# Optimization experiments

Hardware: AMD Instinct MI355X
Metric: run time of the kernel (lower is better)

Reference implementation:

```python
import jax, jax.numpy as jnp
import numpy as np

NUM_HEADS = 8  # attention_head_size = C // NUM_HEADS, used only for score scaling


def conv1x1(x, w, b):
    # x: [B, Cin, H, W], w: [Cout, Cin], b: [Cout]
    return jnp.einsum('bchw,oc->bohw', x, w) + b[None, :, None, None]


def setup_inputs() -> dict:
    key = jax.random.key(0)
    ks = jax.random.split(key, 10)
    B, C, H, W = 8, 256, 96, 96
    x = jax.random.normal(ks[0], (B, C, H, W), dtype=jnp.float32)
    y = jax.random.normal(ks[1], (B, 1, 24, 24), dtype=jnp.float32)
    s = 0.02
    wy = jax.random.normal(ks[2], (C, 1), dtype=jnp.float32) * s
    by = jnp.zeros((C,), dtype=jnp.float32)
    wq = jax.random.normal(ks[3], (C, C), dtype=jnp.float32) * s
    bq = jnp.zeros((C,), dtype=jnp.float32)
    wk = jax.random.normal(ks[4], (C, C), dtype=jnp.float32) * s
    bk = jnp.zeros((C,), dtype=jnp.float32)
    wv = jax.random.normal(ks[5], (C, C), dtype=jnp.float32) * s
    bv = jnp.zeros((C,), dtype=jnp.float32)
    return {'x': x, 'y': y, 'wy': wy, 'by': by, 'wq': wq, 'bq': bq,
            'wk': wk, 'bk': bk, 'wv': wv, 'bv': bv}


def reference(x, y, wy, by, wq, bq, wk, bk, wv, bv):
    B, C, H, W = x.shape
    head_size = C // NUM_HEADS
    # x branch
    xq = conv1x1(x, wq, bq)
    xk = conv1x1(x, wk, bk)
    v = conv1x1(x, wv, bv)
    # y branch: 1 -> C channels, bilinear upsample (align_corners=False == half-pixel)
    y2 = conv1x1(y, wy, by)
    y2 = jax.image.resize(y2, (B, C, H, W), method='bilinear')
    yq = conv1x1(y2, wq, bq)
    yk = conv1x1(y2, wk, bk)
    # gated Q/K
    q = (xq * yq).transpose(0, 2, 1, 3)  # [B, H, C, W]
    k = (xk * yk).transpose(0, 2, 1, 3)
    vt = v.transpose(0, 2, 1, 3)
    # channel attention per spatial row: scores [B, H, C, C]
    scores = jnp.einsum('bhcw,bhdw->bhcd', q, k) / jnp.sqrt(jnp.asarray(head_size, x.dtype))
    probs = jax.nn.softmax(scores, axis=-1)
    out = jnp.einsum('bhcd,bhdw->bhcw', probs, vt)
    return out.transpose(0, 2, 1, 3)  # [B, C, H, W]
```

## Files before the change

kernel.cpp:

```cpp
#include <hip/hip_runtime.h>

typedef __bf16 bf16;
typedef __attribute__((ext_vector_type(8))) __bf16 bf16x8;
typedef __attribute__((ext_vector_type(4))) __bf16 bf16x4;
typedef __attribute__((ext_vector_type(4))) float f32x4;

#define MFMA16(A, B, C) __builtin_amdgcn_mfma_f32_16x16x32_bf16(A, B, C, 0, 0, 0)

__global__ __launch_bounds__(256) void k_prep(
    const float* __restrict__ y, const float* __restrict__ wy, const float* __restrict__ by,
    const float* __restrict__ wq, const float* __restrict__ bq,
    const float* __restrict__ wk, const float* __restrict__ bk,
    const float* __restrict__ wv,
    bf16* __restrict__ wq_bf, bf16* __restrict__ wk_bf, bf16* __restrict__ wv_bf,
    float* __restrict__ yu, float* __restrict__ aq, float* __restrict__ cq,
    float* __restrict__ ak, float* __restrict__ ck)
{
  int blk = blockIdx.x, t = threadIdx.x;
  if (blk < 192) {
    int idx4 = blk * 256 + t;
    int fo = idx4 * 4;
    const float* src; bf16* dst; int off;
    if (fo < 65536)       { src = wq; dst = wq_bf; off = fo; }
    else if (fo < 131072) { src = wk; dst = wk_bf; off = fo - 65536; }
    else                  { src = wv; dst = wv_bf; off = fo - 131072; }
    float4 v = *(const float4*)(src + off);
    bf16x4 o;
    o[0] = (bf16)v.x; o[1] = (bf16)v.y; o[2] = (bf16)v.z; o[3] = (bf16)v.w;
    *(bf16x4*)(dst + off) = o;
  } else if (blk < 200) {
    int b = blk - 192;
    const float* yb = y + b * 576;
#pragma unroll 1
    for (int i = 0; i < 36; ++i) {
      int e = t + i * 256;
      int oh = e / 96, ow = e % 96;
      float sh = oh * 0.25f - 0.375f;
      float sw = ow * 0.25f - 0.375f;
      int ih0 = (int)floorf(sh);
      int iw0 = (int)floorf(sw);
      float fh = sh - (float)ih0, fw = sw - (float)iw0;
      int ih0c = min(23, max(0, ih0)), ih1c = min(23, max(0, ih0 + 1));
      int iw0c = min(23, max(0, iw0)), iw1c = min(23, max(0, iw0 + 1));
      float v00 = yb[ih0c * 24 + iw0c], v01 = yb[ih0c * 24 + iw1c];
      float v10 = yb[ih1c * 24 + iw0c], v11 = yb[ih1c * 24 + iw1c];
      yu[b * 9216 + e] = (1.0f - fh) * ((1.0f - fw) * v00 + fw * v01)
                       + fh * ((1.0f - fw) * v10 + fw * v11);
    }
  } else {
    int ol = t >> 5, cl = t & 31;
    int o = (blk - 200) * 8 + ol;
    int c0 = cl * 8;
    float4 wy0 = *(const float4*)(wy + c0), wy1 = *(const float4*)(wy + c0 + 4);
    float4 by0 = *(const float4*)(by + c0), by1 = *(const float4*)(by + c0 + 4);
    float4 q0  = *(const float4*)(wq + o * 256 + c0), q1 = *(const float4*)(wq + o * 256 + c0 + 4);
    float4 k0  = *(const float4*)(wk + o * 256 + c0), k1 = *(const float4*)(wk + o * 256 + c0 + 4);
    float wyv[8] = {wy0.x, wy0.y, wy0.z, wy0.w, wy1.x, wy1.y, wy1.z, wy1.w};
    float byv[8] = {by0.x, by0.y, by0.z, by0.w, by1.x, by1.y, by1.z, by1.w};
    float qv[8]  = {q0.x, q0.y, q0.z, q0.w, q1.x, q1.y, q1.z, q1.w};
    float kv[8]  = {k0.x, k0.y, k0.z, k0.w, k1.x, k1.y, k1.z, k1.w};
    float saq = 0.f, scq = 0.f, sak = 0.f, sck = 0.f;
#pragma unroll
    for (int j = 0; j < 8; ++j) {
      saq += qv[j] * wyv[j]; scq += qv[j] * byv[j];
      sak += kv[j] * wyv[j]; sck += kv[j] * byv[j];
    }
#pragma unroll
    for (int s = 16; s >= 1; s >>= 1) {
      saq += __shfl_xor(saq, s, 32);
      scq += __shfl_xor(scq, s, 32);
      sak += __shfl_xor(sak, s, 32);
      sck += __shfl_xor(sck, s, 32);
    }
    if (cl == 0) {
      aq[o] = saq; cq[o] = scq + bq[o];
      ak[o] = sak; ck[o] = sck + bk[o];
    }
  }
}

__global__ __launch_bounds__(1024, 1) void k_fused(
    const float* __restrict__ x, const float* __restrict__ yu,
    const bf16* __restrict__ wq_bf, const bf16* __restrict__ wk_bf, const bf16* __restrict__ wv_bf,
    const float* __restrict__ bq, const float* __restrict__ bk, const float* __restrict__ bv,
    const float* __restrict__ aq, const float* __restrict__ cq,
    const float* __restrict__ ak, const float* __restrict__ ck,
    float* __restrict__ out)
{
  __shared__ __align__(16) bf16 xs[96 * 264];
  __shared__ __align__(16) bf16 ks[256 * 104];

  int pl = blockIdx.x;
  int b = pl / 96, h = pl % 96;
  int t = threadIdx.x;
  int wid = t >> 6, lane = t & 63;
  int l15 = lane & 15, g = lane >> 4;
  int otile = wid * 16;

  {
    const float* xrow = x + (size_t)b * 2359296 + (size_t)h * 96;
#pragma unroll
    for (int i = 0; i < 3; ++i) {
      int tsk = i * 1024 + t;
      int w = tsk % 96;
      int c0 = (tsk / 96) * 8;
      float v[8];
#pragma unroll
      for (int j = 0; j < 8; ++j) v[j] = xrow[(size_t)(c0 + j) * 9216 + w];
      bf16x8 o8;
#pragma unroll
      for (int j = 0; j < 8; ++j) o8[j] = (bf16)v[j];
      *(bf16x8*)(xs + w * 264 + c0) = o8;
    }
  }

  size_t wo0 = (size_t)(otile + l15) * 256 + g * 8;
  bf16x8 Bq_c = *(const bf16x8*)(wq_bf + wo0);
  bf16x8 Bk_c = *(const bf16x8*)(wk_bf + wo0);
  bf16x8 Bv_c = *(const bf16x8*)(wv_bf + wo0);

  __syncthreads();

  const float SC = 0.17677669529663687f;

  bf16x8 qf[3];

  {
    f32x4 qacc[6] = {};
    f32x4 kacc[6] = {};
    f32x4 vacc[6] = {};
#pragma unroll 1
    for (int kq = 0; kq < 8; ++kq) {
      bf16x8 Bq_n, Bk_n, Bv_n;
      if (kq < 7) {
        size_t wo = wo0 + (kq + 1) * 32;
        Bq_n = *(const bf16x8*)(wq_bf + wo);
        Bk_n = *(const bf16x8*)(wk_bf + wo);
        Bv_n = *(const bf16x8*)(wv_bf + wo);
      }
      const bf16* xp = xs + kq * 32 + g * 8;
      bf16x8 A[6];
#pragma unroll
      for (int m = 0; m < 6; ++m)
        A[m] = *(const bf16x8*)(xp + (m * 16 + l15) * 264);
#pragma unroll
      for (int m = 0; m < 6; ++m) {
        qacc[m] = MFMA16(A[m], Bq_c, qacc[m]);
        kacc[m] = MFMA16(A[m], Bk_c, kacc[m]);
        vacc[m] = MFMA16(Bv_c, A[m], vacc[m]);
      }
      Bq_c = Bq_n; Bk_c = Bk_n; Bv_c = Bv_n;
    }

    float4 yv[6];
    {
      const float* yr = yu + (size_t)pl * 96;
#pragma unroll
      for (int mt = 0; mt < 6; ++mt)
        yv[mt] = *(const float4*)(yr + mt * 16 + g * 4);
    }
    int o = otile + l15;
    float bqv = bq[o], aq0 = aq[o], cq0 = cq[o];
    float bkv = bk[o], ak0 = ak[o], ck0 = ck[o];

#pragma unroll
    for (int kk = 0; kk < 3; ++kk) {
      bf16x8 qq;
#pragma unroll
      for (int jh = 0; jh < 2; ++jh) {
        int m = 2 * kk + jh;
        float yy[4] = {yv[m].x, yv[m].y, yv[m].z, yv[m].w};
#pragma unroll
        for (int r = 0; r < 4; ++r)
          qq[jh * 4 + r] = (bf16)((qacc[m][r] + bqv) * (yy[r] * aq0 + cq0) * SC);
      }
      qf[kk] = qq;
    }

#pragma unroll
    for (int m = 0; m < 6; ++m) {
      float yy[4] = {yv[m].x, yv[m].y, yv[m].z, yv[m].w};
      bf16x4 pk;
#pragma unroll
      for (int r = 0; r < 4; ++r)
        pk[r] = (bf16)((kacc[m][r] + bkv) * (yy[r] * ak0 + ck0));
      *(bf16x4*)(ks + (size_t)o * 104 + m * 16 + g * 4) = pk;
    }

    float4 bm = *(const float4*)(bv + otile + g * 4);
    float bb[4] = {bm.x, bm.y, bm.z, bm.w};
    __syncthreads();
    bf16* vs = xs;
    int vbase = (otile & ~16) + ((otile >> 2) & 4);
#pragma unroll
    for (int n = 0; n < 6; ++n) {
      bf16x4 pk;
#pragma unroll
      for (int r = 0; r < 4; ++r) pk[r] = (bf16)(vacc[n][r] + bb[r]);
      *(bf16x4*)(vs + (size_t)(n * 16 + l15) * 264 + vbase + g * 8) = pk;
    }
  }
  __syncthreads();

  const bf16* vs = xs;
  f32x4 oacc[6] = {};
  float lp = 0.f;

  auto load_K = [&](int dt, bf16x8* K) {
    const bf16* kp = ks + (size_t)(dt * 32 + l15) * 104 + g * 4;
#pragma unroll
    for (int kk = 0; kk < 3; ++kk)
#pragma unroll
      for (int dn = 0; dn < 2; ++dn) {
        const bf16* p = kp + (size_t)(dn * 16) * 104 + kk * 32;
        bf16x4 lo = *(const bf16x4*)(p);
        bf16x4 hi = *(const bf16x4*)(p + 16);
        K[kk * 2 + dn] = __builtin_shufflevector(lo, hi, 0, 1, 2, 3, 4, 5, 6, 7);
      }
  };

  bf16x8 KA[6], KB[6];
  load_K(0, KA);

  auto attn_step = [&](int dt, bf16x8* Kc, bf16x8* Kn, bool pf) {
    int d0 = dt * 32;
    if (pf) load_K(dt + 1, Kn);
    f32x4 s0 = {}, s1 = {};
    __builtin_amdgcn_s_setprio(1);
#pragma unroll
    for (int kk = 0; kk < 3; ++kk) {
      s0 = MFMA16(Kc[kk * 2 + 0], qf[kk], s0);
      s1 = MFMA16(Kc[kk * 2 + 1], qf[kk], s1);
    }
    __builtin_amdgcn_s_setprio(0);
    bf16x8 pa;
#pragma unroll
    for (int r = 0; r < 4; ++r) {
      float e0 = __expf(s0[r]);
      float e1 = __expf(s1[r]);
      lp += e0 + e1;
      pa[r] = (bf16)e0;
      pa[4 + r] = (bf16)e1;
    }
    const bf16* vp = vs + (size_t)l15 * 264 + d0 + g * 8;
    __builtin_amdgcn_s_setprio(1);
#pragma unroll
    for (int n = 0; n < 6; ++n) {
      bf16x8 Bv = *(const bf16x8*)(vp + (size_t)n * 16 * 264);
      oacc[n] = MFMA16(pa, Bv, oacc[n]);
    }
    __builtin_amdgcn_s_setprio(0);
  };

#pragma unroll 1
  for (int dt2 = 0; dt2 < 4; ++dt2) {
    attn_step(2 * dt2,     KA, KB, true);
    attn_step(2 * dt2 + 1, KB, KA, 2 * dt2 + 1 < 7);
  }

  float vsum = lp;
  vsum += __shfl_xor(vsum, 16, 64);
  vsum += __shfl_xor(vsum, 32, 64);
  float inv = 1.0f / vsum;
  float invr[4];
#pragma unroll
  for (int r = 0; r < 4; ++r)
    invr[r] = __shfl(inv, g * 4 + r, 16);

  float* ob = out + (size_t)b * 2359296 + (size_t)h * 96;
#pragma unroll
  for (int n = 0; n < 6; ++n) {
    int w = n * 16 + l15;
#pragma unroll
    for (int r = 0; r < 4; ++r) {
      int o = otile + g * 4 + r;
      ob[(size_t)o * 9216 + w] = oacc[n][r] * invr[r];
    }
  }
}

extern "C" void kernel_launch(void* const* d_in, const int* in_sizes, int n_in,
                              void* d_out, int out_size, void* d_ws, size_t ws_size,
                              hipStream_t stream) {
  const float* x  = (const float*)d_in[0];
  const float* y  = (const float*)d_in[1];
  const float* wy = (const float*)d_in[2];
  const float* by = (const float*)d_in[3];
  const float* wq = (const float*)d_in[4];
  const float* bq = (const float*)d_in[5];
  const float* wk = (const float*)d_in[6];
  const float* bk = (const float*)d_in[7];
  const float* wv = (const float*)d_in[8];
  const float* bv = (const float*)d_in[9];
  float* out = (float*)d_out;

  char* wsb = (char*)d_ws;
  bf16* wq_bf = (bf16*)(wsb);
  bf16* wk_bf = (bf16*)(wsb + 131072);
  bf16* wv_bf = (bf16*)(wsb + 262144);
  float* yu   = (float*)(wsb + 393216);
  float* aq   = (float*)(wsb + 688128);
  float* cq   = (float*)(wsb + 689152);
  float* ak   = (float*)(wsb + 690176);
  float* ck   = (float*)(wsb + 691200);

  hipLaunchKernelGGL(k_prep, dim3(232), dim3(256), 0, stream,
                     y, wy, by, wq, bq, wk, bk, wv,
                     wq_bf, wk_bf, wv_bf, yu, aq, cq, ak, ck);
  hipLaunchKernelGGL(k_fused, dim3(768), dim3(1024), 0, stream,
                     x, yu, wq_bf, wk_bf, wv_bf, bq, bk, bv,
                     aq, cq, ak, ck, out);
}
```

Baseline: 216.2 us.

## Split x-row staging into halves to overlap global loads with first MFMAs

The fused kernel now loads only the first 128 input channels of the x row into LDS before starting the projection MFMAs. Loads for the second half are issued into registers and stay in flight while the first four k-steps run, then get converted and stored to LDS after a barrier. This hides part of the global-load latency of the strided x gather, at the cost of extra registers in a kernel that already runs one 1024-thread block per CU. The prep kernel is also reshaped so weight conversion does two vectors per thread and the bilinear upsample is spread over 96 blocks instead of 8.

```diff
diff --git a/kernel.cpp b/kernel.cpp
--- a/kernel.cpp
+++ b/kernel.cpp
@@ -17,23 +17,27 @@
     float* __restrict__ ak, float* __restrict__ ck)
 {
   int blk = blockIdx.x, t = threadIdx.x;
-  if (blk < 192) {
-    int idx4 = blk * 256 + t;
-    int fo = idx4 * 4;
-    const float* src; bf16* dst; int off;
-    if (fo < 65536)       { src = wq; dst = wq_bf; off = fo; }
-    else if (fo < 131072) { src = wk; dst = wk_bf; off = fo - 65536; }
-    else                  { src = wv; dst = wv_bf; off = fo - 131072; }
-    float4 v = *(const float4*)(src + off);
-    bf16x4 o;
-    o[0] = (bf16)v.x; o[1] = (bf16)v.y; o[2] = (bf16)v.z; o[3] = (bf16)v.w;
-    *(bf16x4*)(dst + off) = o;
-  } else if (blk < 200) {
-    int b = blk - 192;
+  if (blk < 96) {
+#pragma unroll
+    for (int rep = 0; rep < 2; ++rep) {
+      int idx4 = rep * 24576 + blk * 256 + t;
+      int fo = idx4 * 4;
+      const float* src; bf16* dst; int off;
+      if (fo < 65536)       { src = wq; dst = wq_bf; off = fo; }
+      else if (fo < 131072) { src = wk; dst = wk_bf; off = fo - 65536; }
+      else                  { src = wv; dst = wv_bf; off = fo - 131072; }
+      float4 v = *(const float4*)(src + off);
+      bf16x4 o;
+      o[0] = (bf16)v.x; o[1] = (bf16)v.y; o[2] = (bf16)v.z; o[3] = (bf16)v.w;
+      *(bf16x4*)(dst + off) = o;
+    }
+  } else if (blk < 192) {
+    int blkc = blk - 96;
+    int b = blkc / 12, seg = blkc % 12;
     const float* yb = y + b * 576;
-#pragma unroll 1
-    for (int i = 0; i < 36; ++i) {
-      int e = t + i * 256;
+#pragma unroll
+    for (int i = 0; i < 3; ++i) {
+      int e = seg * 768 + i * 256 + t;
       int oh = e / 96, ow = e % 96;
       float sh = oh * 0.25f - 0.375f;
       float sw = ow * 0.25f - 0.375f;
@@ -49,7 +53,7 @@
     }
   } else {
     int ol = t >> 5, cl = t & 31;
-    int o = (blk - 200) * 8 + ol;
+    int o = (blk - 192) * 8 + ol;
     int c0 = cl * 8;
     float4 wy0 = *(const float4*)(wy + c0), wy1 = *(const float4*)(wy + c0 + 4);
     float4 by0 = *(const float4*)(by + c0), by1 = *(const float4*)(by + c0 + 4);
@@ -97,13 +101,14 @@
   int l15 = lane & 15, g = lane >> 4;
   int otile = wid * 16;
 
-  {
-    const float* xrow = x + (size_t)b * 2359296 + (size_t)h * 96;
-#pragma unroll
-    for (int i = 0; i < 3; ++i) {
-      int tsk = i * 1024 + t;
-      int w = tsk % 96;
-      int c0 = (tsk / 96) * 8;
+  const float* xrow = x + (size_t)b * 2359296 + (size_t)h * 96;
+
+#pragma unroll
+  for (int rep = 0; rep < 2; ++rep) {
+    int task = rep * 1024 + t;
+    if (task < 1536) {
+      int w = task % 96;
+      int c0 = (task / 96) * 8;
       float v[8];
 #pragma unroll
       for (int j = 0; j < 8; ++j) v[j] = xrow[(size_t)(c0 + j) * 9216 + w];
@@ -129,8 +134,57 @@
     f32x4 qacc[6] = {};
     f32x4 kacc[6] = {};
     f32x4 vacc[6] = {};
+
+    float vB0[8], vB1[8];
+    int wB0 = t % 96, cB0 = (t / 96) * 8 + 128;
+#pragma unroll
+    for (int j = 0; j < 8; ++j) vB0[j] = xrow[(size_t)(cB0 + j) * 9216 + wB0];
+    int tB1 = 1024 + t;
+    int wB1 = tB1 % 96, cB1 = (tB1 / 96) * 8 + 128;
+    if (t < 512) {
+#pragma unroll
+      for (int j = 0; j < 8; ++j) vB1[j] = xrow[(size_t)(cB1 + j) * 9216 + wB1];
+    }
+
 #pragma unroll 1
-    for (int kq = 0; kq < 8; ++kq) {
+    for (int kq = 0; kq < 4; ++kq) {
+      bf16x8 Bq_n, Bk_n, Bv_n;
+      {
+        size_t wo = wo0 + (kq + 1) * 32;
+        Bq_n = *(const bf16x8*)(wq_bf + wo);
+        Bk_n = *(const bf16x8*)(wk_bf + wo);
+        Bv_n = *(const bf16x8*)(wv_bf + wo);
+      }
+      const bf16* xp = xs + kq * 32 + g * 8;
+      bf16x8 A[6];
+#pragma unroll
+      for (int m = 0; m < 6; ++m)
+        A[m] = *(const bf16x8*)(xp + (m * 16 + l15) * 264);
+#pragma unroll
+      for (int m = 0; m < 6; ++m) {
+        qacc[m] = MFMA16(A[m], Bq_c, qacc[m]);
+        kacc[m] = MFMA16(A[m], Bk_c, kacc[m]);
+        vacc[m] = MFMA16(Bv_c, A[m], vacc[m]);
+      }
+      Bq_c = Bq_n; Bk_c = Bk_n; Bv_c = Bv_n;
+    }
+
+    {
+      bf16x8 o8;
+#pragma unroll
+      for (int j = 0; j < 8; ++j) o8[j] = (bf16)vB0[j];
+      *(bf16x8*)(xs + wB0 * 264 + cB0) = o8;
+      if (t < 512) {
+        bf16x8 o9;
+#pragma unroll
+        for (int j = 0; j < 8; ++j) o9[j] = (bf16)vB1[j];
+        *(bf16x8*)(xs + wB1 * 264 + cB1) = o9;
+      }
+    }
+    __syncthreads();
+
+#pragma unroll 1
+    for (int kq = 4; kq < 8; ++kq) {
       bf16x8 Bq_n, Bk_n, Bv_n;
       if (kq < 7) {
         size_t wo = wo0 + (kq + 1) * 32;
@@ -304,7 +358,7 @@
   float* ak   = (float*)(wsb + 690176);
   float* ck   = (float*)(wsb + 691200);
 
-  hipLaunchKernelGGL(k_prep, dim3(232), dim3(256), 0, stream,
+  hipLaunchKernelGGL(k_prep, dim3(224), dim3(256), 0, stream,
                      y, wy, by, wq, bq, wk, bk, wv,
                      wq_bf, wk_bf, wv_bf, yu, aq, cq, ak, ck);
   hipLaunchKernelGGL(k_fused, dim3(768), dim3(1024), 0, stream,
```

Measured after the change: 212.4 us. Within noise of the previous version (-1.7%).

## Stagger per-wave K-loop start offsets and rebalance prep kernel block partition

Applied to the files above, without the earlier changes.

Each wave starts its weight-K loop and attention d-tile loop at a rotated offset (s8 derived from wave id), so different waves read different LDS and global rows at the same moment. This aims to cut LDS bank conflicts and contention on the weight loads. The prep kernel is also repartitioned: the weight-cast blocks each handle two chunks, and the bilinear upsample is split across 96 blocks instead of 8, which should shorten that kernel's critical path. The rotation is order-only, so results change only through floating-point summation order.

```diff
diff --git a/kernel.cpp b/kernel.cpp
--- a/kernel.cpp
+++ b/kernel.cpp
@@ -17,23 +17,27 @@
     float* __restrict__ ak, float* __restrict__ ck)
 {
   int blk = blockIdx.x, t = threadIdx.x;
-  if (blk < 192) {
-    int idx4 = blk * 256 + t;
-    int fo = idx4 * 4;
-    const float* src; bf16* dst; int off;
-    if (fo < 65536)       { src = wq; dst = wq_bf; off = fo; }
-    else if (fo < 131072) { src = wk; dst = wk_bf; off = fo - 65536; }
-    else                  { src = wv; dst = wv_bf; off = fo - 131072; }
-    float4 v = *(const float4*)(src + off);
-    bf16x4 o;
-    o[0] = (bf16)v.x; o[1] = (bf16)v.y; o[2] = (bf16)v.z; o[3] = (bf16)v.w;
-    *(bf16x4*)(dst + off) = o;
-  } else if (blk < 200) {
-    int b = blk - 192;
+  if (blk < 96) {
+#pragma unroll
+    for (int rep = 0; rep < 2; ++rep) {
+      int idx4 = rep * 24576 + blk * 256 + t;
+      int fo = idx4 * 4;
+      const float* src; bf16* dst; int off;
+      if (fo < 65536)       { src = wq; dst = wq_bf; off = fo; }
+      else if (fo < 131072) { src = wk; dst = wk_bf; off = fo - 65536; }
+      else                  { src = wv; dst = wv_bf; off = fo - 131072; }
+      float4 v = *(const float4*)(src + off);
+      bf16x4 o;
+      o[0] = (bf16)v.x; o[1] = (bf16)v.y; o[2] = (bf16)v.z; o[3] = (bf16)v.w;
+      *(bf16x4*)(dst + off) = o;
+    }
+  } else if (blk < 192) {
+    int blkc = blk - 96;
+    int b = blkc / 12, seg = blkc % 12;
     const float* yb = y + b * 576;
-#pragma unroll 1
-    for (int i = 0; i < 36; ++i) {
-      int e = t + i * 256;
+#pragma unroll
+    for (int i = 0; i < 3; ++i) {
+      int e = seg * 768 + i * 256 + t;
       int oh = e / 96, ow = e % 96;
       float sh = oh * 0.25f - 0.375f;
       float sw = ow * 0.25f - 0.375f;
@@ -49,7 +53,7 @@
     }
   } else {
     int ol = t >> 5, cl = t & 31;
-    int o = (blk - 200) * 8 + ol;
+    int o = (blk - 192) * 8 + ol;
     int c0 = cl * 8;
     float4 wy0 = *(const float4*)(wy + c0), wy1 = *(const float4*)(wy + c0 + 4);
     float4 by0 = *(const float4*)(by + c0), by1 = *(const float4*)(by + c0 + 4);
@@ -96,28 +100,28 @@
   int wid = t >> 6, lane = t & 63;
   int l15 = lane & 15, g = lane >> 4;
   int otile = wid * 16;
-
-  {
-    const float* xrow = x + (size_t)b * 2359296 + (size_t)h * 96;
-#pragma unroll
-    for (int i = 0; i < 3; ++i) {
-      int tsk = i * 1024 + t;
-      int w = tsk % 96;
-      int c0 = (tsk / 96) * 8;
-      float v[8];
-#pragma unroll
-      for (int j = 0; j < 8; ++j) v[j] = xrow[(size_t)(c0 + j) * 9216 + w];
-      bf16x8 o8;
-#pragma unroll
-      for (int j = 0; j < 8; ++j) o8[j] = (bf16)v[j];
-      *(bf16x8*)(xs + w * 264 + c0) = o8;
-    }
+  int s8 = (wid + (wid >> 2)) & 7;
+
+  const float* xrow = x + (size_t)b * 2359296 + (size_t)h * 96;
+
+#pragma unroll
+  for (int i = 0; i < 3; ++i) {
+    int tsk = i * 1024 + t;
+    int w = tsk % 96;
+    int c0 = (tsk / 96) * 8;
+    float v[8];
+#pragma unroll
+    for (int j = 0; j < 8; ++j) v[j] = xrow[(size_t)(c0 + j) * 9216 + w];
+    bf16x8 o8;
+#pragma unroll
+    for (int j = 0; j < 8; ++j) o8[j] = (bf16)v[j];
+    *(bf16x8*)(xs + w * 264 + c0) = o8;
   }
 
   size_t wo0 = (size_t)(otile + l15) * 256 + g * 8;
-  bf16x8 Bq_c = *(const bf16x8*)(wq_bf + wo0);
-  bf16x8 Bk_c = *(const bf16x8*)(wk_bf + wo0);
-  bf16x8 Bv_c = *(const bf16x8*)(wv_bf + wo0);
+  bf16x8 Bq_c = *(const bf16x8*)(wq_bf + wo0 + s8 * 32);
+  bf16x8 Bk_c = *(const bf16x8*)(wk_bf + wo0 + s8 * 32);
+  bf16x8 Bv_c = *(const bf16x8*)(wv_bf + wo0 + s8 * 32);
 
   __syncthreads();
 
@@ -130,10 +134,11 @@
     f32x4 kacc[6] = {};
     f32x4 vacc[6] = {};
 #pragma unroll 1
-    for (int kq = 0; kq < 8; ++kq) {
+    for (int i = 0; i < 8; ++i) {
+      int kq = (s8 + i) & 7;
       bf16x8 Bq_n, Bk_n, Bv_n;
-      if (kq < 7) {
-        size_t wo = wo0 + (kq + 1) * 32;
+      if (i < 7) {
+        size_t wo = wo0 + (size_t)(((s8 + i + 1) & 7) * 32);
         Bq_n = *(const bf16x8*)(wq_bf + wo);
         Bk_n = *(const bf16x8*)(wk_bf + wo);
         Bv_n = *(const bf16x8*)(wv_bf + wo);
@@ -220,11 +225,11 @@
   };
 
   bf16x8 KA[6], KB[6];
-  load_K(0, KA);
+  load_K(s8, KA);
 
   auto attn_step = [&](int dt, bf16x8* Kc, bf16x8* Kn, bool pf) {
     int d0 = dt * 32;
-    if (pf) load_K(dt + 1, Kn);
+    if (pf) load_K((dt + 1) & 7, Kn);
     f32x4 s0 = {}, s1 = {};
     __builtin_amdgcn_s_setprio(1);
 #pragma unroll
@@ -253,9 +258,9 @@
   };
 
 #pragma unroll 1
-  for (int dt2 = 0; dt2 < 4; ++dt2) {
-    attn_step(2 * dt2,     KA, KB, true);
-    attn_step(2 * dt2 + 1, KB, KA, 2 * dt2 + 1 < 7);
+  for (int i2 = 0; i2 < 4; ++i2) {
+    attn_step((s8 + 2 * i2) & 7,     KA, KB, true);
+    attn_step((s8 + 2 * i2 + 1) & 7, KB, KA, 2 * i2 + 1 < 7);
   }
 
   float vsum = lp;
@@ -304,7 +309,7 @@
   float* ak   = (float*)(wsb + 690176);
   float* ck   = (float*)(wsb + 691200);
 
-  hipLaunchKernelGGL(k_prep, dim3(232), dim3(256), 0, stream,
+  hipLaunchKernelGGL(k_prep, dim3(224), dim3(256), 0, stream,
                      y, wy, by, wq, bq, wk, bk, wv,
                      wq_bf, wk_bf, wv_bf, yu, aq, cq, ak, ck);
   hipLaunchKernelGGL(k_fused, dim3(768), dim3(1024), 0, stream,
```

Measured after the change: 211.5 us. 2.2% less time.
